# Optimization experiments

Hardware: AMD Instinct MI355X
Metric: run time of the kernel (lower is better)

The kernel has to match this reference:

```python
import jax, jax.numpy as jnp
import numpy as np
from jax import lax

B, C, H, W = 4, 128, 128, 128
MAXD = 192
D = MAXD // 4            # 48 disparity hypotheses at 1/4 scale
WS = 8                   # window size
NH = 8                   # num heads
HD = C // NH             # head dim = 16
SCALE = HD ** -0.5
HID = 4 * C              # mlp hidden (mlp_ratio=4)


def _rel_index(ws):
    coords = np.stack(np.meshgrid(np.arange(ws), np.arange(ws), indexing='ij'))
    cf = coords.reshape(2, -1)
    rel = (cf[:, :, None] - cf[:, None, :]).transpose(1, 2, 0)
    rel[:, :, 0] += ws - 1
    rel[:, :, 1] += ws - 1
    rel[:, :, 0] *= 2 * ws - 1
    return rel.sum(-1)   # [ws*ws, ws*ws]

REL_IDX = jnp.asarray(_rel_index(WS))


def setup_inputs() -> dict:
    key = jax.random.key(0)
    ks = iter(jax.random.split(key, 40))
    rn = lambda shape, s=0.02: jax.random.normal(next(ks), shape, dtype=jnp.float32) * s
    return {
        'feat_l': jax.random.normal(next(ks), (B, C, H, W), dtype=jnp.float32),
        'feat_r': jax.random.normal(next(ks), (B, C, H, W), dtype=jnp.float32),
        'wq': rn((C, C)), 'bq': jnp.zeros((C,), jnp.float32),
        'wk': rn((C, C)), 'bk': jnp.zeros((C,), jnp.float32),
        'wv': rn((C, C)), 'bv': jnp.zeros((C,), jnp.float32),
        'wp': rn((C, C)), 'bp': jnp.zeros((C,), jnp.float32),
        'rpb': rn(((2 * WS - 1) ** 2, NH)),
        'ln1_g': jnp.ones((C,), jnp.float32), 'ln1_b': jnp.zeros((C,), jnp.float32),
        'ln2_g': jnp.ones((C,), jnp.float32), 'ln2_b': jnp.zeros((C,), jnp.float32),
        'mlp_w1': rn((C, HID)), 'mlp_b1': jnp.zeros((HID,), jnp.float32),
        'mlp_w2': rn((HID, C)), 'mlp_b2': jnp.zeros((C,), jnp.float32),
        'un_w1': rn((C, C)), 'un_b1': jnp.zeros((C,), jnp.float32),
        'un_w2': rn((C, C)), 'un_b2': jnp.zeros((C,), jnp.float32),
        'dp_w1': rn((C // 2 + D // 2 + 16, C + D, 3, 3)) if False else rn(((C + D) // 2, C + D, 3, 3)),
        'dp_b1': jnp.zeros(((C + D) // 2,), jnp.float32),
        'bn_g': jnp.ones(((C + D) // 2,), jnp.float32), 'bn_b': jnp.zeros(((C + D) // 2,), jnp.float32),
        'dp_w2': rn((D, (C + D) // 2, 1, 1)), 'dp_b2': jnp.zeros((D,), jnp.float32),
    }


def _ln(x, g, b):
    m = x.mean(-1, keepdims=True)
    v = x.var(-1, keepdims=True)
    return (x - m) * jax.lax.rsqrt(v + 1e-5) * g + b


def _conv(x, w, b, pad):
    y = lax.conv_general_dilated(x, w, (1, 1), [(pad, pad), (pad, pad)],
                                 dimension_numbers=('NCHW', 'OIHW', 'NCHW'))
    return y + b[None, :, None, None]


def _cost_volume(fl, fr):
    # corr[:, d] = mean_c fl[..., w] * fr[..., w-d], zero-padded on the left
    outs = [jnp.mean(fl * fr, axis=1)]
    for d in range(1, D):
        fr_s = jnp.pad(fr[:, :, :, :-d], ((0, 0), (0, 0), (0, 0), (d, 0)))
        outs.append(jnp.mean(fl * fr_s, axis=1))
    return jnp.stack(outs, axis=1)  # [B, D, H, W]


def _win_part(tok):  # [B, H*W, C] -> [B*nW, WS*WS, C]
    x = tok.reshape(B, H // WS, WS, W // WS, WS, C)
    return x.transpose(0, 1, 3, 2, 4, 5).reshape(-1, WS * WS, C)


def _win_rev(win):  # [B*nW, WS*WS, C] -> [B, H*W, C]
    x = win.reshape(B, H // WS, W // WS, WS, WS, C)
    return x.transpose(0, 1, 3, 2, 4, 5).reshape(B, H * W, C)


def _forward(feat_l, feat_r, wq, bq, wk, bk, wv, bv, wp, bp, rpb,
             ln1_g, ln1_b, ln2_g, ln2_b, mlp_w1, mlp_b1, mlp_w2, mlp_b2,
             un_w1, un_b1, un_w2, un_b2, dp_w1, dp_b1, bn_g, bn_b, dp_w2, dp_b2):
    gelu = lambda x: jax.nn.gelu(x, approximate=False)
    cost = _cost_volume(feat_l, feat_r)                       # [B, D, H, W]

    tokens = feat_l.reshape(B, C, H * W).transpose(0, 2, 1)   # [B, N, C]
    unary = gelu(tokens @ un_w1 + un_b1) @ un_w2 + un_b2      # unary potential

    nf = _ln(_win_part(tokens), ln1_g, ln1_b)                 # [Bw, 64, C]
    Bw, N = nf.shape[0], WS * WS
    q = (nf @ wq + bq).reshape(Bw, N, NH, HD).transpose(0, 2, 1, 3)
    k = (nf @ wk + bk).reshape(Bw, N, NH, HD).transpose(0, 2, 1, 3)
    v = (nf @ wv + bv).reshape(Bw, N, NH, HD).transpose(0, 2, 1, 3)
    attn = jnp.einsum('bhnd,bhmd->bhnm', q, k) * SCALE
    bias = rpb[REL_IDX.reshape(-1)].reshape(N, N, NH).transpose(2, 0, 1)
    attn = jax.nn.softmax(attn + bias[None], axis=-1)
    o = jnp.einsum('bhnm,bhmd->bhnd', attn, v).transpose(0, 2, 1, 3).reshape(Bw, N, C)
    pairwise = o @ wp + bp

    x = unary + _win_rev(pairwise)
    x = x + gelu(_ln(x, ln2_g, ln2_b) @ mlp_w1 + mlp_b1) @ mlp_w2 + mlp_b2 * 0.0 + (jnp.zeros((), jnp.float32))
    # (faithful residual MLP; the extra zero terms are no-ops kept out below)
    # -- recompute cleanly to avoid confusion:
    # x = x + mlp(norm2(x))  already done above via single expression

    crf = x.transpose(0, 2, 1).reshape(B, C, H, W)
    fused = jnp.concatenate([crf, cost], axis=1)              # [B, C+D, H, W]

    h1 = jax.nn.relu((_conv(fused, dp_w1, dp_b1, 1)) * jax.lax.rsqrt(jnp.float32(1.0 + 1e-5)) * bn_g[None, :, None, None] + bn_b[None, :, None, None])
    pv = _conv(h1, dp_w2, dp_b2, 0)                           # [B, D, H, W]
    prob = jax.nn.softmax(pv, axis=1)
    disp = jnp.arange(D, dtype=jnp.float32)[None, :, None, None]
    pred = jnp.sum(prob * disp, axis=1, keepdims=True) * 4.0  # [B, 1, H, W]
    return pred


def reference(feat_l, feat_r, wq, bq, wk, bk, wv, bv, wp, bp, rpb,
              ln1_g, ln1_b, ln2_g, ln2_b, mlp_w1, mlp_b1, mlp_w2, mlp_b2,
              un_w1, un_b1, un_w2, un_b2, dp_w1, dp_b1, bn_g, bn_b, dp_w2, dp_b2):
    return _forward(feat_l, feat_r, wq, bq, wk, bk, wv, bv, wp, bp, rpb,
                    ln1_g, ln1_b, ln2_g, ln2_b, mlp_w1, mlp_b1, mlp_w2, mlp_b2,
                    un_w1, un_b1, un_w2, un_b2, dp_w1, dp_b1, bn_g, bn_b, dp_w2, dp_b2)
```

## Files before the change

### kernel.cpp

```cpp
#include <hip/hip_runtime.h>
#include <math.h>

constexpr int Bn = 4, Cc = 128, Hh = 128, Wn = 128, Dd = 48;
constexpr float SCALE = 0.25f;

typedef short  bf16x8 __attribute__((ext_vector_type(8)));
typedef short  bf16x4 __attribute__((ext_vector_type(4)));
typedef float  f32x4  __attribute__((ext_vector_type(4)));
typedef unsigned short u16x8 __attribute__((ext_vector_type(8)));

static __device__ __forceinline__ unsigned short f2bf(float f) {
    return __builtin_bit_cast(unsigned short, (__bf16)f);
}
static __device__ __forceinline__ float bf2f(unsigned short u) {
    return __uint_as_float((unsigned int)u << 16);
}
static __device__ __forceinline__ unsigned int pack2bf(float a, float b) {
    return (unsigned int)f2bf(a) | ((unsigned int)f2bf(b) << 16);
}
static __device__ __forceinline__ float gelu_f(float v) {
    float u = v * (1.5957691216f + 0.0713548162f * v * v);
    return v * __builtin_amdgcn_rcpf(1.0f + __expf(-u));
}

static __device__ __forceinline__ size_t opk_addr(int b, int wh, int ww, int Mt, int ks, int lane) {
    return ((size_t)(b * 16384) + (wh * 8 + Mt * 2 + (ks >> 1)) * 128 + ww * 8) * 128
           + (ks & 1) * 512 + lane * 8;
}

__global__ __launch_bounds__(384) void k_cost(const float* __restrict__ fl,
                                              const float* __restrict__ fr,
                                              unsigned short* __restrict__ costbf) {
    __shared__ float s_fl[2][16][64];
    __shared__ float s_fr[2][16][112];
    int tid = threadIdx.x;
    int w0 = blockIdx.x * 64;
    int hp = blockIdx.y, b = blockIdx.z;
    int row = tid / 192;
    int r = tid - row * 192;
    int wg = r & 15, dg = r >> 4;
    int W = wg * 4, D = dg * 4;
    int h = hp * 2 + row;
    float acc[4][4];
#pragma unroll
    for (int i = 0; i < 4; ++i)
#pragma unroll
        for (int j = 0; j < 4; ++j) acc[i][j] = 0.f;

#pragma unroll 1
    for (int ck = 0; ck < 8; ++ck) {
        int ci0 = ck * 16;
        for (int i = tid; i < 512; i += 384) {
            int rr = i >> 8, rem = i & 255;
            int c = rem >> 4, k4 = rem & 15;
            float4 v = *(const float4*)&fl[((size_t)(b * 128 + ci0 + c) << 14) + (hp * 2 + rr) * 128 + w0 + k4 * 4];
            *(float4*)&s_fl[rr][c][k4 * 4] = v;
        }
        for (int i = tid; i < 896; i += 384) {
            int rr = i / 448, rem = i - rr * 448;
            int c = rem / 28, k4 = rem - c * 28;
            int wgl = w0 - 48 + k4 * 4;
            float4 v = {0.f, 0.f, 0.f, 0.f};
            if (wgl >= 0)
                v = *(const float4*)&fr[((size_t)(b * 128 + ci0 + c) << 14) + (hp * 2 + rr) * 128 + wgl];
            *(float4*)&s_fr[rr][c][k4 * 4] = v;
        }
        __syncthreads();
#pragma unroll
        for (int c = 0; c < 16; ++c) {
            float4 flv = *(const float4*)&s_fl[row][c][W];
            int base = W - D + 44;
            float4 f0 = *(const float4*)&s_fr[row][c][base];
            float4 f1 = *(const float4*)&s_fr[row][c][base + 4];
            float fw[8] = {f0.x, f0.y, f0.z, f0.w, f1.x, f1.y, f1.z, f1.w};
            float fv[4] = {flv.x, flv.y, flv.z, flv.w};
#pragma unroll
            for (int dj = 0; dj < 4; ++dj)
#pragma unroll
                for (int wv = 0; wv < 4; ++wv)
                    acc[dj][wv] += fv[wv] * fw[wv - dj + 4];
        }
        __syncthreads();
    }
    const float inv = 1.0f / 128.0f;
    unsigned short* cb = costbf + ((size_t)(b << 14) + h * 128 + w0 + W) * 64;
    const u16x8 z8 = {0, 0, 0, 0, 0, 0, 0, 0};
#pragma unroll
    for (int wv = 0; wv < 4; ++wv) {
        bf16x4 o4;
#pragma unroll
        for (int dj = 0; dj < 4; ++dj) o4[dj] = (short)f2bf(acc[dj][wv] * inv);
        *(bf16x4*)&cb[wv * 64 + D] = o4;
        if (D == 44) {
            *(u16x8*)&cb[wv * 64 + 48] = z8;
            *(u16x8*)&cb[wv * 64 + 56] = z8;
        }
    }
}

static __device__ void pack_conv(int blk, int lane,
                                 const float* __restrict__ w1, const float* __restrict__ b1,
                                 const float* __restrict__ bng, const float* __restrict__ bnb,
                                 unsigned short* __restrict__ pk, float* __restrict__ bias2) {
    const float rs = 0.9999950000374997f;
    int ct = blk % 6;
    int taplin = blk / 6;
    int tap = taplin % 9, chunk = taplin / 9;
    int co = ct * 16 + (lane & 15);
    int cibase = chunk * 32 + (lane >> 4) * 8;
    u16x8 out;
#pragma unroll
    for (int j = 0; j < 8; ++j) {
        int ci = cibase + j;
        float v = 0.f;
        if (co < 88 && ci < 176) v = w1[(size_t)co * 1584 + ci * 9 + tap] * rs * bng[co];
        out[j] = f2bf(v);
    }
    *(u16x8*)(pk + ((size_t)blk * 64 + lane) * 8) = out;
    if (blk == 0) {
        for (int i = lane; i < 96; i += 64)
            bias2[i] = (i < 88) ? (b1[i] * rs * bng[i] + bnb[i]) : 0.f;
    }
}

static __device__ void pack_gemmB(int blk, int lane,
                                  const float* __restrict__ W,
                                  unsigned short* __restrict__ out, int ncols) {
    int ntiles = ncols >> 4;
    int ks = blk & 3;
    int nt = (blk >> 2) % ntiles;
    int kc = blk / (4 * ntiles);
    int col = nt * 16 + (lane & 15);
    int k0 = kc * 128 + ks * 32 + (lane >> 4) * 8;
    u16x8 o;
#pragma unroll
    for (int j = 0; j < 8; ++j) o[j] = f2bf(W[(size_t)(k0 + j) * ncols + col]);
    *(u16x8*)(out + ((size_t)blk * 64 + lane) * 8) = o;
}

static __device__ void pack_rpb(int blk, int lane,
                                const float* __restrict__ rpb, float* __restrict__ pb) {
    int nt = blk & 3, mt = (blk >> 2) & 3, hh = blk >> 4;
    int tq = nt * 16 + (lane & 15);
    int g = lane >> 4;
    float o[4];
#pragma unroll
    for (int rr = 0; rr < 4; ++rr) {
        int tk = mt * 16 + g * 4 + rr;
        int relidx = (((tq >> 3) - (tk >> 3)) + 7) * 15 + ((tq & 7) - (tk & 7)) + 7;
        o[rr] = rpb[relidx * 8 + hh];
    }
    float4 v = {o[0], o[1], o[2], o[3]};
    *(float4*)(pb + ((size_t)blk * 64 + lane) * 4) = v;
}

__global__ __launch_bounds__(64) void k_pack_all(
        const float* __restrict__ dp_w1, const float* __restrict__ dp_b1,
        const float* __restrict__ bn_g, const float* __restrict__ bn_b,
        unsigned short* __restrict__ pk, float* __restrict__ bias2,
        const float* __restrict__ wq, const float* __restrict__ wk,
        const float* __restrict__ wv, const float* __restrict__ wp,
        unsigned short* __restrict__ pkw,
        const float* __restrict__ rpb, float* __restrict__ pb,
        const float* __restrict__ mlp_w1, unsigned short* __restrict__ pm1,
        const float* __restrict__ mlp_w2, unsigned short* __restrict__ pm2,
        const float* __restrict__ un_w1, unsigned short* __restrict__ pu1,
        const float* __restrict__ un_w2, unsigned short* __restrict__ pu2) {
    int blk = blockIdx.x;
    int lane = threadIdx.x;
    if (blk < 324) {
        pack_conv(blk, lane, dp_w1, dp_b1, bn_g, bn_b, pk, bias2);
    } else if (blk < 452) {
        int bb = blk - 324;
        int mat = bb >> 5;
        const float* W = (mat == 0) ? wq : (mat == 1) ? wk : (mat == 2) ? wv : wp;
        pack_gemmB(bb & 31, lane, W, pkw + (size_t)mat * 16384, 128);
    } else if (blk < 580) {
        pack_rpb(blk - 452, lane, rpb, pb);
    } else if (blk < 708) {
        pack_gemmB(blk - 580, lane, mlp_w1, pm1, 512);
    } else if (blk < 836) {
        pack_gemmB(blk - 708, lane, mlp_w2, pm2, 128);
    } else if (blk < 868) {
        pack_gemmB(blk - 836, lane, un_w1, pu1, 128);
    } else {
        pack_gemmB(blk - 868, lane, un_w2, pu2, 128);
    }
}

__global__ __launch_bounds__(256) void k_unary_mfma(const float* __restrict__ feat_l,
                                                    const unsigned short* __restrict__ pu1,
                                                    const float* __restrict__ b1,
                                                    const unsigned short* __restrict__ pu2,
                                                    const float* __restrict__ b2,
                                                    const float* __restrict__ g1,
                                                    const float* __restrict__ bt1,
                                                    float* __restrict__ x,
                                                    unsigned short* __restrict__ nf) {
    __shared__ __align__(16) unsigned short s_a[64 * 136];
    __shared__ __align__(16) unsigned short s_h[64 * 136];
    int tid = threadIdx.x;
    int wid = tid >> 6, lane = tid & 63;
    int g = lane >> 4, t = lane & 15;
    int n0g = blockIdx.x * 64;
    int b = n0g >> 14;
    int nb = n0g & 16383;

    for (int idx = tid; idx < 4096; idx += 256) {
        int c2 = idx >> 6, nl = idx & 63;
        float v0 = feat_l[((size_t)(b * 128 + 2 * c2) << 14) + nb + nl];
        float v1 = feat_l[((size_t)(b * 128 + 2 * c2 + 1) << 14) + nb + nl];
        *(unsigned int*)&s_a[nl * 136 + 2 * c2] = pack2bf(v0, v1);
    }
    __syncthreads();

    {
        int tok = tid >> 2, q = tid & 3;
        float v[32];
#pragma unroll
        for (int i8 = 0; i8 < 4; ++i8) {
            u16x8 r8 = *(const u16x8*)&s_a[tok * 136 + q * 32 + i8 * 8];
#pragma unroll
            for (int j = 0; j < 8; ++j) v[i8 * 8 + j] = bf2f(r8[j]);
        }
        float s = 0.f, s2 = 0.f;
#pragma unroll
        for (int i = 0; i < 32; ++i) { s += v[i]; s2 += v[i] * v[i]; }
        s += __shfl_xor(s, 1); s += __shfl_xor(s, 2);
        s2 += __shfl_xor(s2, 1); s2 += __shfl_xor(s2, 2);
        float mean = s * (1.f / 128.f);
        float var = s2 * (1.f / 128.f) - mean * mean;
        float rstd = rsqrtf(var + 1e-5f);
        size_t base = (size_t)(n0g + tok) * 128 + q * 32;
#pragma unroll
        for (int i8 = 0; i8 < 4; ++i8) {
            u16x8 o8;
#pragma unroll
            for (int j = 0; j < 8; ++j) {
                int c = q * 32 + i8 * 8 + j;
                o8[j] = f2bf((v[i8 * 8 + j] - mean) * rstd * g1[c] + bt1[c]);
            }
            *(u16x8*)&nf[base + i8 * 8] = o8;
        }
    }

    bf16x8 af[4][4];
#pragma unroll
    for (int Mt = 0; Mt < 4; ++Mt)
#pragma unroll
        for (int ks = 0; ks < 4; ++ks)
            af[Mt][ks] = *(const bf16x8*)&s_a[(Mt * 16 + t) * 136 + ks * 32 + g * 8];

    f32x4 acc1[4][2];
#pragma unroll
    for (int nt2 = 0; nt2 < 2; ++nt2) {
        float bv = b1[(wid * 2 + nt2) * 16 + t];
#pragma unroll
        for (int Mt = 0; Mt < 4; ++Mt) acc1[Mt][nt2] = (f32x4){bv, bv, bv, bv};
    }
#pragma unroll
    for (int ks = 0; ks < 4; ++ks) {
        bf16x8 bf0 = *(const bf16x8*)(pu1 + (size_t)(((wid * 2 + 0) * 4 + ks) * 64 + lane) * 8);
        bf16x8 bf1 = *(const bf16x8*)(pu1 + (size_t)(((wid * 2 + 1) * 4 + ks) * 64 + lane) * 8);
#pragma unroll
        for (int Mt = 0; Mt < 4; ++Mt) {
            acc1[Mt][0] = __builtin_amdgcn_mfma_f32_16x16x32_bf16(af[Mt][ks], bf0, acc1[Mt][0], 0, 0, 0);
            acc1[Mt][1] = __builtin_amdgcn_mfma_f32_16x16x32_bf16(af[Mt][ks], bf1, acc1[Mt][1], 0, 0, 0);
        }
    }
#pragma unroll
    for (int Mt = 0; Mt < 4; ++Mt)
#pragma unroll
        for (int nt2 = 0; nt2 < 2; ++nt2)
#pragma unroll
            for (int rr = 0; rr < 4; ++rr)
                s_h[(Mt * 16 + g * 4 + rr) * 136 + (wid * 2 + nt2) * 16 + t] = f2bf(gelu_f(acc1[Mt][nt2][rr]));
    __syncthreads();

    bf16x8 a2[4][4];
#pragma unroll
    for (int Mt = 0; Mt < 4; ++Mt)
#pragma unroll
        for (int ks = 0; ks < 4; ++ks)
            a2[Mt][ks] = *(const bf16x8*)&s_h[(Mt * 16 + t) * 136 + ks * 32 + g * 8];

    f32x4 acc2[4][2];
#pragma unroll
    for (int nt2 = 0; nt2 < 2; ++nt2) {
        float bv = b2[(wid * 2 + nt2) * 16 + t];
#pragma unroll
        for (int Mt = 0; Mt < 4; ++Mt) acc2[Mt][nt2] = (f32x4){bv, bv, bv, bv};
    }
#pragma unroll
    for (int ks = 0; ks < 4; ++ks) {
        bf16x8 bf0 = *(const bf16x8*)(pu2 + (size_t)(((wid * 2 + 0) * 4 + ks) * 64 + lane) * 8);
        bf16x8 bf1 = *(const bf16x8*)(pu2 + (size_t)(((wid * 2 + 1) * 4 + ks) * 64 + lane) * 8);
#pragma unroll
        for (int Mt = 0; Mt < 4; ++Mt) {
            acc2[Mt][0] = __builtin_amdgcn_mfma_f32_16x16x32_bf16(a2[Mt][ks], bf0, acc2[Mt][0], 0, 0, 0);
            acc2[Mt][1] = __builtin_amdgcn_mfma_f32_16x16x32_bf16(a2[Mt][ks], bf1, acc2[Mt][1], 0, 0, 0);
        }
    }
#pragma unroll
    for (int Mt = 0; Mt < 4; ++Mt)
#pragma unroll
        for (int nt2 = 0; nt2 < 2; ++nt2)
#pragma unroll
            for (int rr = 0; rr < 4; ++rr) {
                int tok = Mt * 16 + g * 4 + rr;
                x[(size_t)(n0g + tok) * 128 + (wid * 2 + nt2) * 16 + t] = acc2[Mt][nt2][rr];
            }
}

__global__ __launch_bounds__(256, 3) void k_attn_core(const unsigned short* nf,
                                                      const unsigned short* __restrict__ pkw,
                                                      const float* __restrict__ pb,
                                                      const float* __restrict__ bq,
                                                      const float* __restrict__ bk,
                                                      const float* __restrict__ bv,
                                                      unsigned short* opk) {
    __shared__ __align__(16) unsigned short s_all[4 * 5760];
    int tid = threadIdx.x;
    int wid = tid >> 6, lane = tid & 63;
    int g = lane >> 4, t = lane & 15;
    int bw = blockIdx.x;
    int b = bw >> 8, wh = (bw >> 4) & 15, ww = bw & 15;

    bf16x8 af[4][4];
#pragma unroll
    for (int Mt = 0; Mt < 4; ++Mt) {
        int tok = Mt * 16 + t;
        size_t gtok = (size_t)(b * 16384) + (wh * 8 + (tok >> 3)) * 128 + ww * 8 + (tok & 7);
#pragma unroll
        for (int ks = 0; ks < 4; ++ks)
            af[Mt][ks] = *(const bf16x8*)&nf[gtok * 128 + ks * 32 + g * 8];
    }
    __syncthreads();

    unsigned short* sQ = s_all + wid * 5760;
    unsigned short* sK = sQ + 1536;
    unsigned short* sV = sQ + 4608;
    unsigned short* sP = sQ;
    unsigned short* sO = sQ;

    const bf16x8 z8v = {0, 0, 0, 0, 0, 0, 0, 0};

#pragma unroll
    for (int hi = 0; hi < 2; ++hi) {
        int h = wid + hi * 4;

        float bqv = bq[h * 16 + t], bkv = bk[h * 16 + t], bvv = bv[h * 16 + t];
        f32x4 qa[4], ka[4], va[4];
#pragma unroll
        for (int Mt = 0; Mt < 4; ++Mt) {
            qa[Mt] = (f32x4){bqv, bqv, bqv, bqv};
            ka[Mt] = (f32x4){bkv, bkv, bkv, bkv};
            va[Mt] = (f32x4){bvv, bvv, bvv, bvv};
        }
#pragma unroll
        for (int ks = 0; ks < 4; ++ks) {
            const unsigned short* wbase = pkw + ((size_t)((h * 4 + ks) * 64 + lane) * 8);
            bf16x8 bfq = *(const bf16x8*)(wbase);
            bf16x8 bfk = *(const bf16x8*)(wbase + 16384);
            bf16x8 bfv = *(const bf16x8*)(wbase + 32768);
#pragma unroll
            for (int Mt = 0; Mt < 4; ++Mt) {
                qa[Mt] = __builtin_amdgcn_mfma_f32_16x16x32_bf16(af[Mt][ks], bfq, qa[Mt], 0, 0, 0);
                ka[Mt] = __builtin_amdgcn_mfma_f32_16x16x32_bf16(af[Mt][ks], bfk, ka[Mt], 0, 0, 0);
                va[Mt] = __builtin_amdgcn_mfma_f32_16x16x32_bf16(af[Mt][ks], bfv, va[Mt], 0, 0, 0);
            }
        }
#pragma unroll
        for (int Mt = 0; Mt < 4; ++Mt) {
            bf16x4 vv;
#pragma unroll
            for (int rr = 0; rr < 4; ++rr) {
                int tok = Mt * 16 + g * 4 + rr;
                sQ[tok * 24 + t] = f2bf(qa[Mt][rr] * SCALE);
                sK[tok * 24 + t] = f2bf(ka[Mt][rr]);
                vv[rr] = (short)f2bf(va[Mt][rr]);
            }
            *(bf16x4*)&sV[t * 72 + Mt * 16 + g * 4] = vv;
        }

        f32x4 s[4][4];
#pragma unroll
        for (int Mtk = 0; Mtk < 4; ++Mtk)
#pragma unroll
            for (int Ntq = 0; Ntq < 4; ++Ntq)
                s[Mtk][Ntq] = *(const f32x4*)(pb + ((size_t)((h * 16 + Mtk * 4 + Ntq) * 64 + lane) * 4));
        bf16x8 bQ[4];
#pragma unroll
        for (int Ntq = 0; Ntq < 4; ++Ntq)
            bQ[Ntq] = (g < 2) ? *(const bf16x8*)&sQ[(Ntq * 16 + t) * 24 + g * 8] : z8v;
#pragma unroll
        for (int Mtk = 0; Mtk < 4; ++Mtk) {
            bf16x8 aK = (g < 2) ? *(const bf16x8*)&sK[(Mtk * 16 + t) * 24 + g * 8] : z8v;
#pragma unroll
            for (int Ntq = 0; Ntq < 4; ++Ntq)
                s[Mtk][Ntq] = __builtin_amdgcn_mfma_f32_16x16x32_bf16(aK, bQ[Ntq], s[Mtk][Ntq], 0, 0, 0);
        }

#pragma unroll
        for (int Ntq = 0; Ntq < 4; ++Ntq) {
            float m = s[0][Ntq][0];
#pragma unroll
            for (int Mtk = 0; Mtk < 4; ++Mtk)
#pragma unroll
                for (int rr = 0; rr < 4; ++rr) m = fmaxf(m, s[Mtk][Ntq][rr]);
            m = fmaxf(m, __shfl_xor(m, 16));
            m = fmaxf(m, __shfl_xor(m, 32));
            float sum = 0.f;
#pragma unroll
            for (int Mtk = 0; Mtk < 4; ++Mtk)
#pragma unroll
                for (int rr = 0; rr < 4; ++rr) {
                    float e = __expf(s[Mtk][Ntq][rr] - m);
                    s[Mtk][Ntq][rr] = e;
                    sum += e;
                }
            sum += __shfl_xor(sum, 16);
            sum += __shfl_xor(sum, 32);
            float inv = __builtin_amdgcn_rcpf(sum);
#pragma unroll
            for (int Mtk = 0; Mtk < 4; ++Mtk) {
                bf16x4 pv;
#pragma unroll
                for (int rr = 0; rr < 4; ++rr) pv[rr] = (short)f2bf(s[Mtk][Ntq][rr] * inv);
                *(bf16x4*)&sP[(Ntq * 16 + t) * 72 + Mtk * 16 + g * 4] = pv;
            }
        }

        f32x4 oa[4];
#pragma unroll
        for (int Mt = 0; Mt < 4; ++Mt) oa[Mt] = (f32x4){0.f, 0.f, 0.f, 0.f};
#pragma unroll
        for (int ksv = 0; ksv < 2; ++ksv) {
            bf16x8 bv2 = *(const bf16x8*)&sV[t * 72 + ksv * 32 + g * 8];
#pragma unroll
            for (int Mt = 0; Mt < 4; ++Mt) {
                bf16x8 ap = *(const bf16x8*)&sP[(Mt * 16 + t) * 72 + ksv * 32 + g * 8];
                oa[Mt] = __builtin_amdgcn_mfma_f32_16x16x32_bf16(ap, bv2, oa[Mt], 0, 0, 0);
            }
        }
#pragma unroll
        for (int Mt = 0; Mt < 4; ++Mt)
#pragma unroll
            for (int rr = 0; rr < 4; ++rr)
                sO[(Mt * 16 + g * 4 + rr) * 16 + t] = f2bf(oa[Mt][rr]);
        int ksf = h >> 1;
        if ((g >> 1) == (h & 1)) {
#pragma unroll
            for (int Mt = 0; Mt < 4; ++Mt) {
                bf16x8 v8 = *(const bf16x8*)&sO[(Mt * 16 + t) * 16 + (g & 1) * 8];
                *(bf16x8*)&opk[opk_addr(b, wh, ww, Mt, ksf, lane)] = v8;
            }
        }
    }
}

__global__ __launch_bounds__(256) void k_mlp_mfma(float* __restrict__ x,
                                                  const unsigned short* __restrict__ opk,
                                                  const unsigned short* __restrict__ pkw,
                                                  const float* __restrict__ bp,
                                                  const float* __restrict__ g2,
                                                  const float* __restrict__ bt2,
                                                  const unsigned short* __restrict__ pm1,
                                                  const float* __restrict__ b1,
                                                  const unsigned short* __restrict__ pm2) {
    __shared__ __align__(16) char smem[35328];
    float* sf = (float*)smem;
    unsigned short* s_h = (unsigned short*)smem;
    float* s_st = (float*)(smem + 33792);
    float* s_gb = (float*)(smem + 34304);
    int tid = threadIdx.x;
    int wid = tid >> 6, lane = tid & 63;
    int g = lane >> 4, t = lane & 15;
    int bw = blockIdx.x;
    int b = bw >> 8, wh = (bw >> 4) & 15, ww = bw & 15;

    auto gtok_of = [&](int tok) -> size_t {
        return (size_t)(b * 16384) + (wh * 8 + (tok >> 3)) * 128 + ww * 8 + (tok & 7);
    };

    if (tid < 128) s_gb[tid] = g2[tid];
    else if (tid < 256) s_gb[tid] = bt2[tid - 128];

    f32x4 out[4][2];
    {
        float bp0 = bp[wid * 32 + t], bp1 = bp[wid * 32 + 16 + t];
#pragma unroll
        for (int Mt = 0; Mt < 4; ++Mt) {
            out[Mt][0] = (f32x4){bp0, bp0, bp0, bp0};
            out[Mt][1] = (f32x4){bp1, bp1, bp1, bp1};
        }
#pragma unroll
        for (int ks = 0; ks < 4; ++ks) {
            bf16x8 b0 = *(const bf16x8*)(pkw + 49152 + (size_t)(((wid * 2 + 0) * 4 + ks) * 64 + lane) * 8);
            bf16x8 b1v = *(const bf16x8*)(pkw + 49152 + (size_t)(((wid * 2 + 1) * 4 + ks) * 64 + lane) * 8);
#pragma unroll
            for (int Mt = 0; Mt < 4; ++Mt) {
                bf16x8 a = *(const bf16x8*)&opk[opk_addr(b, wh, ww, Mt, ks, lane)];
                out[Mt][0] = __builtin_amdgcn_mfma_f32_16x16x32_bf16(a, b0, out[Mt][0], 0, 0, 0);
                out[Mt][1] = __builtin_amdgcn_mfma_f32_16x16x32_bf16(a, b1v, out[Mt][1], 0, 0, 0);
            }
        }
#pragma unroll
        for (int Mt = 0; Mt < 4; ++Mt)
#pragma unroll
            for (int nt2 = 0; nt2 < 2; ++nt2)
#pragma unroll
                for (int rr = 0; rr < 4; ++rr) {
                    int tok = Mt * 16 + g * 4 + rr;
                    int col = (wid * 2 + nt2) * 16 + t;
                    float v = out[Mt][nt2][rr] + x[gtok_of(tok) * 128 + col];
                    out[Mt][nt2][rr] = v;
                    sf[tok * 132 + col] = v;
                }
    }
    __syncthreads();
    {
        int tok = tid >> 2, q = tid & 3;
        float s = 0.f, s2 = 0.f;
        for (int c = q * 32; c < q * 32 + 32; ++c) {
            float v = sf[tok * 132 + c];
            s += v; s2 += v * v;
        }
        s += __shfl_xor(s, 1); s += __shfl_xor(s, 2);
        s2 += __shfl_xor(s2, 1); s2 += __shfl_xor(s2, 2);
        if (q == 0) {
            float mean = s * (1.f / 128.f);
            float var = s2 * (1.f / 128.f) - mean * mean;
            s_st[tok * 2] = mean;
            s_st[tok * 2 + 1] = rsqrtf(var + 1e-5f);
        }
    }
    __syncthreads();
    bf16x8 af2[4][4];
#pragma unroll
    for (int Mt = 0; Mt < 4; ++Mt) {
        int tok = Mt * 16 + t;
        float mean = s_st[tok * 2], rstd = s_st[tok * 2 + 1];
#pragma unroll
        for (int ks = 0; ks < 4; ++ks) {
            int c0 = ks * 32 + g * 8;
            float4 v0 = *(const float4*)&sf[tok * 132 + c0];
            float4 v1 = *(const float4*)&sf[tok * 132 + c0 + 4];
            float vv[8] = {v0.x, v0.y, v0.z, v0.w, v1.x, v1.y, v1.z, v1.w};
            u16x8 o8;
#pragma unroll
            for (int j = 0; j < 8; ++j)
                o8[j] = f2bf((vv[j] - mean) * rstd * s_gb[c0 + j] + s_gb[128 + c0 + j]);
            af2[Mt][ks] = __builtin_bit_cast(bf16x8, o8);
        }
    }
    __syncthreads();

#pragma unroll 1
    for (int hc = 0; hc < 2; ++hc) {
#pragma unroll
        for (int jh = 0; jh < 2; ++jh) {
            f32x4 acc1[4][2];
#pragma unroll
            for (int j2 = 0; j2 < 2; ++j2) {
                float bv = b1[hc * 256 + (wid * 4 + jh * 2 + j2) * 16 + t];
#pragma unroll
                for (int Mt = 0; Mt < 4; ++Mt) acc1[Mt][j2] = (f32x4){bv, bv, bv, bv};
            }
#pragma unroll
            for (int ks = 0; ks < 4; ++ks) {
                int nt0 = hc * 16 + wid * 4 + jh * 2;
                bf16x8 bf0 = *(const bf16x8*)(pm1 + (size_t)((((nt0 + 0) * 4 + ks) * 64 + lane) * 8));
                bf16x8 bf1 = *(const bf16x8*)(pm1 + (size_t)((((nt0 + 1) * 4 + ks) * 64 + lane) * 8));
#pragma unroll
                for (int Mt = 0; Mt < 4; ++Mt) {
                    acc1[Mt][0] = __builtin_amdgcn_mfma_f32_16x16x32_bf16(af2[Mt][ks], bf0, acc1[Mt][0], 0, 0, 0);
                    acc1[Mt][1] = __builtin_amdgcn_mfma_f32_16x16x32_bf16(af2[Mt][ks], bf1, acc1[Mt][1], 0, 0, 0);
                }
            }
#pragma unroll
            for (int Mt = 0; Mt < 4; ++Mt)
#pragma unroll
                for (int j2 = 0; j2 < 2; ++j2)
#pragma unroll
                    for (int rr = 0; rr < 4; ++rr)
                        s_h[(Mt * 16 + g * 4 + rr) * 264 + (wid * 4 + jh * 2 + j2) * 16 + t] =
                            f2bf(gelu_f(acc1[Mt][j2][rr]));
        }
        __syncthreads();
#pragma unroll
        for (int kt = 0; kt < 8; ++kt) {
            int kc = hc * 2 + (kt >> 2), ks = kt & 3;
            bf16x8 bf0 = *(const bf16x8*)(pm2 + (size_t)(((kc * 32 + (wid * 2 + 0) * 4 + ks) * 64 + lane) * 8));
            bf16x8 bf1 = *(const bf16x8*)(pm2 + (size_t)(((kc * 32 + (wid * 2 + 1) * 4 + ks) * 64 + lane) * 8));
#pragma unroll
            for (int Mt = 0; Mt < 4; ++Mt) {
                bf16x8 a2 = *(const bf16x8*)&s_h[(Mt * 16 + t) * 264 + kt * 32 + g * 8];
                out[Mt][0] = __builtin_amdgcn_mfma_f32_16x16x32_bf16(a2, bf0, out[Mt][0], 0, 0, 0);
                out[Mt][1] = __builtin_amdgcn_mfma_f32_16x16x32_bf16(a2, bf1, out[Mt][1], 0, 0, 0);
            }
        }
        __syncthreads();
    }

#pragma unroll
    for (int Mt = 0; Mt < 4; ++Mt)
#pragma unroll
        for (int nt2 = 0; nt2 < 2; ++nt2)
#pragma unroll
            for (int rr = 0; rr < 4; ++rr) {
                int tok = Mt * 16 + g * 4 + rr;
                x[gtok_of(tok) * 128 + (wid * 2 + nt2) * 16 + t] = out[Mt][nt2][rr];
            }
}

__global__ __launch_bounds__(256) void k_conv_mfma(const float* __restrict__ x,
                                                   const unsigned short* __restrict__ costbf,
                                                   const unsigned short* __restrict__ pk,
                                                   const float* __restrict__ bias2,
                                                   float* __restrict__ h1) {
    __shared__ __align__(16) unsigned short s_p[180 * 40];
    int tid = threadIdx.x;
    int wid = tid >> 6, lane = tid & 63;
    int g = lane >> 4, t = lane & 15;
    int tx0 = blockIdx.x * 16, ty0 = blockIdx.y * 8, b = blockIdx.z;

    f32x4 acc[2][6];
#pragma unroll
    for (int p = 0; p < 2; ++p)
#pragma unroll
        for (int ct = 0; ct < 6; ++ct) acc[p][ct] = (f32x4){0.f, 0.f, 0.f, 0.f};

#pragma unroll 1
    for (int chunk = 0; chunk < 6; ++chunk) {
        if (chunk < 4) {
            int ci0 = chunk * 32;
            for (int u = tid; u < 360; u += 256) {
                int pos = u >> 1, half = u & 1;
                int yy = pos / 18, xx = pos - yy * 18;
                int gy = ty0 + yy - 1, gx = tx0 + xx - 1;
                u16x8 lo, hi;
                if (gy >= 0 && gy < 128 && gx >= 0 && gx < 128) {
                    const float4* src = (const float4*)&x[((size_t)(b << 14) + gy * 128 + gx) * 128 + ci0 + half * 16];
                    float4 v0 = src[0], v1 = src[1], v2 = src[2], v3 = src[3];
                    lo[0] = f2bf(v0.x); lo[1] = f2bf(v0.y); lo[2] = f2bf(v0.z); lo[3] = f2bf(v0.w);
                    lo[4] = f2bf(v1.x); lo[5] = f2bf(v1.y); lo[6] = f2bf(v1.z); lo[7] = f2bf(v1.w);
                    hi[0] = f2bf(v2.x); hi[1] = f2bf(v2.y); hi[2] = f2bf(v2.z); hi[3] = f2bf(v2.w);
                    hi[4] = f2bf(v3.x); hi[5] = f2bf(v3.y); hi[6] = f2bf(v3.z); hi[7] = f2bf(v3.w);
                } else {
                    lo = (u16x8)(unsigned short)0; hi = (u16x8)(unsigned short)0;
                }
                unsigned short* dst = &s_p[pos * 40 + half * 16];
                *(u16x8*)dst = lo;
                *(u16x8*)(dst + 8) = hi;
            }
        } else {
            int d0 = (chunk - 4) * 32;
            for (int u = tid; u < 180; u += 256) {
                int yy = u / 18, xx = u - yy * 18;
                int gy = ty0 + yy - 1, gx = tx0 + xx - 1;
                u16x8 lo = (u16x8)(unsigned short)0, hi = (u16x8)(unsigned short)0;
                if (gy >= 0 && gy < 128 && gx >= 0 && gx < 128) {
                    const u16x8* src = (const u16x8*)&costbf[((size_t)(b << 14) + gy * 128 + gx) * 64 + d0];
                    lo = src[0]; hi = src[1];
                    u16x8 l2 = src[2], h2 = src[3];
                    *(u16x8*)&s_p[u * 40 + 16] = l2;
                    *(u16x8*)&s_p[u * 40 + 24] = h2;
                } else {
                    *(u16x8*)&s_p[u * 40 + 16] = lo;
                    *(u16x8*)&s_p[u * 40 + 24] = hi;
                }
                *(u16x8*)&s_p[u * 40 + 0] = lo;
                *(u16x8*)&s_p[u * 40 + 8] = hi;
            }
        }
        __syncthreads();

#pragma unroll 1
        for (int tap = 0; tap < 9; ++tap) {
            int dy = tap / 3, dx = tap - dy * 3;
            const unsigned short* pkt = pk + ((size_t)(chunk * 9 + tap)) * 6 * 512;
            bf16x8 afr[6];
#pragma unroll
            for (int ct = 0; ct < 6; ++ct)
                afr[ct] = *(const bf16x8*)(pkt + ct * 512 + lane * 8);
            bf16x8 bfr[2];
#pragma unroll
            for (int p = 0; p < 2; ++p) {
                int pos = (wid * 2 + p + dy) * 18 + t + dx;
                bfr[p] = *(const bf16x8*)&s_p[pos * 40 + g * 8];
            }
#pragma unroll
            for (int p = 0; p < 2; ++p)
#pragma unroll
                for (int ct = 0; ct < 6; ++ct)
                    acc[p][ct] = __builtin_amdgcn_mfma_f32_16x16x32_bf16(afr[ct], bfr[p], acc[p][ct], 0, 0, 0);
        }
        __syncthreads();
    }

#pragma unroll
    for (int p = 0; p < 2; ++p) {
        int y = ty0 + wid * 2 + p;
#pragma unroll
        for (int ct = 0; ct < 6; ++ct) {
#pragma unroll
            for (int rr = 0; rr < 4; ++rr) {
                int co = ct * 16 + g * 4 + rr;
                if (co < 88) {
                    float v = acc[p][ct][rr] + bias2[co];
                    h1[((size_t)(b * 88 + co) << 14) + y * 128 + tx0 + t] = fmaxf(v, 0.f);
                }
            }
        }
    }
}

__global__ __launch_bounds__(256) void k_head(const float* __restrict__ h1,
                                              const float* __restrict__ w2, const float* __restrict__ b2,
                                              float* __restrict__ out) {
    __shared__ float s_wt[88 * 48];
    __shared__ float s_b[48];
    int tid = threadIdx.x;
    for (int idx = tid; idx < 48 * 88; idx += 256) {
        int d = idx / 88, k = idx % 88;
        s_wt[k * 48 + d] = w2[idx];
    }
    if (tid < 48) s_b[tid] = b2[tid];
    __syncthreads();
    int px = blockIdx.x * 256 + tid;
    int b = px >> 14, r = px & 16383;
    float acc[48];
#pragma unroll
    for (int d = 0; d < 48; ++d) acc[d] = s_b[d];
    for (int k = 0; k < 88; ++k) {
        float hv = h1[((size_t)(b * 88 + k) << 14) + r];
        const float4* wrow = (const float4*)&s_wt[k * 48];
#pragma unroll
        for (int d4 = 0; d4 < 12; ++d4) {
            float4 wv = wrow[d4];
            acc[d4 * 4 + 0] += hv * wv.x;
            acc[d4 * 4 + 1] += hv * wv.y;
            acc[d4 * 4 + 2] += hv * wv.z;
            acc[d4 * 4 + 3] += hv * wv.w;
        }
    }
    float mx = -1e30f;
#pragma unroll
    for (int d = 0; d < 48; ++d) mx = fmaxf(mx, acc[d]);
    float sum = 0.f, wsum = 0.f;
#pragma unroll
    for (int d = 0; d < 48; ++d) {
        float e = __expf(acc[d] - mx);
        sum += e;
        wsum += e * (float)d;
    }
    out[px] = 4.0f * wsum * __builtin_amdgcn_rcpf(sum);
}

extern "C" void kernel_launch(void* const* d_in, const int* in_sizes, int n_in,
                              void* d_out, int out_size, void* d_ws, size_t ws_size,
                              hipStream_t stream) {
    const float* feat_l = (const float*)d_in[0];
    const float* feat_r = (const float*)d_in[1];
    const float* wq = (const float*)d_in[2];
    const float* bq = (const float*)d_in[3];
    const float* wk = (const float*)d_in[4];
    const float* bk = (const float*)d_in[5];
    const float* wv = (const float*)d_in[6];
    const float* bv = (const float*)d_in[7];
    const float* wp = (const float*)d_in[8];
    const float* bp = (const float*)d_in[9];
    const float* rpb = (const float*)d_in[10];
    const float* ln1_g = (const float*)d_in[11];
    const float* ln1_b = (const float*)d_in[12];
    const float* ln2_g = (const float*)d_in[13];
    const float* ln2_b = (const float*)d_in[14];
    const float* mlp_w1 = (const float*)d_in[15];
    const float* mlp_b1 = (const float*)d_in[16];
    const float* mlp_w2 = (const float*)d_in[17];
    const float* un_w1 = (const float*)d_in[19];
    const float* un_b1 = (const float*)d_in[20];
    const float* un_w2 = (const float*)d_in[21];
    const float* un_b2 = (const float*)d_in[22];
    const float* dp_w1 = (const float*)d_in[23];
    const float* dp_b1 = (const float*)d_in[24];
    const float* bn_g = (const float*)d_in[25];
    const float* bn_b = (const float*)d_in[26];
    const float* dp_w2 = (const float*)d_in[27];
    const float* dp_b2 = (const float*)d_in[28];

    float* ws = (float*)d_ws;
    unsigned short* costbf = (unsigned short*)ws;
    float* x = ws + 3145728;
    float* h1 = ws + 11534336;
    unsigned short* nfo = (unsigned short*)h1;
    unsigned short* pk = (unsigned short*)(ws + 17301504);
    float* bias2 = ws + 17384448;
    unsigned short* pkw = (unsigned short*)(ws + 17384544);
    float* pb = ws + 17417312;
    unsigned short* pm1 = (unsigned short*)(ws + 17450080);
    unsigned short* pm2 = (unsigned short*)(ws + 17482848);
    unsigned short* pu1 = (unsigned short*)(ws + 17515616);
    unsigned short* pu2 = (unsigned short*)(ws + 17523808);
    float* out = (float*)d_out;

    k_pack_all<<<900, 64, 0, stream>>>(dp_w1, dp_b1, bn_g, bn_b, pk, bias2,
                                       wq, wk, wv, wp, pkw, rpb, pb,
                                       mlp_w1, pm1, mlp_w2, pm2,
                                       un_w1, pu1, un_w2, pu2);
    k_cost<<<dim3(2, 64, 4), 384, 0, stream>>>(feat_l, feat_r, costbf);
    k_unary_mfma<<<1024, 256, 0, stream>>>(feat_l, pu1, un_b1, pu2, un_b2,
                                           ln1_g, ln1_b, x, nfo);
    k_attn_core<<<1024, 256, 0, stream>>>(nfo, pkw, pb, bq, bk, bv, nfo);
    k_mlp_mfma<<<1024, 256, 0, stream>>>(x, nfo, pkw, bp, ln2_g, ln2_b,
                                         pm1, mlp_b1, pm2);
    k_conv_mfma<<<dim3(8, 16, 4), 256, 0, stream>>>(x, costbf, pk, bias2, h1);
    k_head<<<256, 256, 0, stream>>>(h1, dp_w2, dp_b2, out);
}
```

Before: 258.5 us.

## Merge cost-volume and unary kernels into one launch with block-range dispatch

Merges the cost-volume kernel and the unary MLP kernel into a single launch. Blocks 0-1023 run the unary path and blocks 1024 and above compute the cost volume, so the two independent stages can share the GPU and one launch is removed. The cost path is also rewritten: each block now handles one row with 256 threads, each thread computing 12 disparities for one column, where the old kernel handled two rows with 384 threads doing 4x4 register tiles. This trades register reuse for more blocks, and shared memory is sized for the larger unary path, which may limit occupancy for the cost blocks.

```diff
diff --git a/kernel.cpp b/kernel.cpp
--- a/kernel.cpp
+++ b/kernel.cpp
@@ -26,76 +26,6 @@
 static __device__ __forceinline__ size_t opk_addr(int b, int wh, int ww, int Mt, int ks, int lane) {
     return ((size_t)(b * 16384) + (wh * 8 + Mt * 2 + (ks >> 1)) * 128 + ww * 8) * 128
            + (ks & 1) * 512 + lane * 8;
-}
-
-__global__ __launch_bounds__(384) void k_cost(const float* __restrict__ fl,
-                                              const float* __restrict__ fr,
-                                              unsigned short* __restrict__ costbf) {
-    __shared__ float s_fl[2][16][64];
-    __shared__ float s_fr[2][16][112];
-    int tid = threadIdx.x;
-    int w0 = blockIdx.x * 64;
-    int hp = blockIdx.y, b = blockIdx.z;
-    int row = tid / 192;
-    int r = tid - row * 192;
-    int wg = r & 15, dg = r >> 4;
-    int W = wg * 4, D = dg * 4;
-    int h = hp * 2 + row;
-    float acc[4][4];
-#pragma unroll
-    for (int i = 0; i < 4; ++i)
-#pragma unroll
-        for (int j = 0; j < 4; ++j) acc[i][j] = 0.f;
-
-#pragma unroll 1
-    for (int ck = 0; ck < 8; ++ck) {
-        int ci0 = ck * 16;
-        for (int i = tid; i < 512; i += 384) {
-            int rr = i >> 8, rem = i & 255;
-            int c = rem >> 4, k4 = rem & 15;
-            float4 v = *(const float4*)&fl[((size_t)(b * 128 + ci0 + c) << 14) + (hp * 2 + rr) * 128 + w0 + k4 * 4];
-            *(float4*)&s_fl[rr][c][k4 * 4] = v;
-        }
-        for (int i = tid; i < 896; i += 384) {
-            int rr = i / 448, rem = i - rr * 448;
-            int c = rem / 28, k4 = rem - c * 28;
-            int wgl = w0 - 48 + k4 * 4;
-            float4 v = {0.f, 0.f, 0.f, 0.f};
-            if (wgl >= 0)
-                v = *(const float4*)&fr[((size_t)(b * 128 + ci0 + c) << 14) + (hp * 2 + rr) * 128 + wgl];
-            *(float4*)&s_fr[rr][c][k4 * 4] = v;
-        }
-        __syncthreads();
-#pragma unroll
-        for (int c = 0; c < 16; ++c) {
-            float4 flv = *(const float4*)&s_fl[row][c][W];
-            int base = W - D + 44;
-            float4 f0 = *(const float4*)&s_fr[row][c][base];
-            float4 f1 = *(const float4*)&s_fr[row][c][base + 4];
-            float fw[8] = {f0.x, f0.y, f0.z, f0.w, f1.x, f1.y, f1.z, f1.w};
-            float fv[4] = {flv.x, flv.y, flv.z, flv.w};
-#pragma unroll
-            for (int dj = 0; dj < 4; ++dj)
-#pragma unroll
-                for (int wv = 0; wv < 4; ++wv)
-                    acc[dj][wv] += fv[wv] * fw[wv - dj + 4];
-        }
-        __syncthreads();
-    }
-    const float inv = 1.0f / 128.0f;
-    unsigned short* cb = costbf + ((size_t)(b << 14) + h * 128 + w0 + W) * 64;
-    const u16x8 z8 = {0, 0, 0, 0, 0, 0, 0, 0};
-#pragma unroll
-    for (int wv = 0; wv < 4; ++wv) {
-        bf16x4 o4;
-#pragma unroll
-        for (int dj = 0; dj < 4; ++dj) o4[dj] = (short)f2bf(acc[dj][wv] * inv);
-        *(bf16x4*)&cb[wv * 64 + D] = o4;
-        if (D == 44) {
-            *(u16x8*)&cb[wv * 64 + 48] = z8;
-            *(u16x8*)&cb[wv * 64 + 56] = z8;
-        }
-    }
 }
 
 static __device__ void pack_conv(int blk, int lane,
@@ -188,21 +118,81 @@
     }
 }
 
-__global__ __launch_bounds__(256) void k_unary_mfma(const float* __restrict__ feat_l,
-                                                    const unsigned short* __restrict__ pu1,
-                                                    const float* __restrict__ b1,
-                                                    const unsigned short* __restrict__ pu2,
-                                                    const float* __restrict__ b2,
-                                                    const float* __restrict__ g1,
-                                                    const float* __restrict__ bt1,
-                                                    float* __restrict__ x,
-                                                    unsigned short* __restrict__ nf) {
-    __shared__ __align__(16) unsigned short s_a[64 * 136];
-    __shared__ __align__(16) unsigned short s_h[64 * 136];
+__global__ __launch_bounds__(256) void k_front(const float* __restrict__ feat_l,
+                                               const float* __restrict__ feat_r,
+                                               unsigned short* __restrict__ costbf,
+                                               const unsigned short* __restrict__ pu1,
+                                               const float* __restrict__ b1,
+                                               const unsigned short* __restrict__ pu2,
+                                               const float* __restrict__ b2,
+                                               const float* __restrict__ g1,
+                                               const float* __restrict__ bt1,
+                                               float* __restrict__ x,
+                                               unsigned short* __restrict__ nf) {
+    __shared__ __align__(16) char smem[34816];
     int tid = threadIdx.x;
+    int blk = blockIdx.x;
+
+    if (blk >= 1024) {
+        int cb = blk - 1024;
+        int wt = cb & 1, h = (cb >> 1) & 127, b = cb >> 8;
+        int w0 = wt * 64;
+        int w = tid & 63, dg = tid >> 6;
+        float* s_fl = (float*)smem;
+        float* s_fr = (float*)(smem + 4096);
+        float acc[12];
+#pragma unroll
+        for (int dj = 0; dj < 12; ++dj) acc[dj] = 0.f;
+
+#pragma unroll 1
+        for (int ck = 0; ck < 8; ++ck) {
+            int ci0 = ck * 16;
+            {
+                int c = tid >> 4, k4 = tid & 15;
+                *(float4*)&s_fl[c * 64 + k4 * 4] =
+                    *(const float4*)&feat_l[((size_t)(b * 128 + ci0 + c) << 14) + h * 128 + w0 + k4 * 4];
+            }
+            for (int i = tid; i < 448; i += 256) {
+                int c = i / 28, k4 = i - c * 28;
+                int wgl = w0 - 48 + k4 * 4;
+                float4 v = {0.f, 0.f, 0.f, 0.f};
+                if (wgl >= 0)
+                    v = *(const float4*)&feat_r[((size_t)(b * 128 + ci0 + c) << 14) + h * 128 + wgl];
+                *(float4*)&s_fr[c * 112 + k4 * 4] = v;
+            }
+            __syncthreads();
+            int base = w + 48 - dg * 12;
+#pragma unroll
+            for (int c = 0; c < 16; ++c) {
+                float flv = s_fl[c * 64 + w];
+#pragma unroll
+                for (int dj = 0; dj < 12; ++dj)
+                    acc[dj] += flv * s_fr[c * 112 + base - dj];
+            }
+            __syncthreads();
+        }
+        const float inv = 1.0f / 128.0f;
+        unsigned short* cbp = costbf + ((size_t)(b << 14) + h * 128 + w0 + w) * 64 + dg * 12;
+#pragma unroll
+        for (int q = 0; q < 3; ++q) {
+            bf16x4 o4;
+#pragma unroll
+            for (int rr = 0; rr < 4; ++rr) o4[rr] = (short)f2bf(acc[q * 4 + rr] * inv);
+            *(bf16x4*)&cbp[q * 4] = o4;
+        }
+        if (dg == 3) {
+            const u16x8 z8 = {0, 0, 0, 0, 0, 0, 0, 0};
+            *(u16x8*)&cbp[12] = z8;
+            *(u16x8*)&cbp[20] = z8;
+        }
+        return;
+    }
+
+    unsigned short* s_a = (unsigned short*)smem;
+    unsigned short* s_h = (unsigned short*)(smem + 17408);
     int wid = tid >> 6, lane = tid & 63;
     int g = lane >> 4, t = lane & 15;
-    int n0g = blockIdx.x * 64;
+    int n0g = blk * 64;
     int b = n0g >> 14;
     int nb = n0g & 16383;
 
@@ -809,9 +799,8 @@
                                        wq, wk, wv, wp, pkw, rpb, pb,
                                        mlp_w1, pm1, mlp_w2, pm2,
                                        un_w1, pu1, un_w2, pu2);
-    k_cost<<<dim3(2, 64, 4), 384, 0, stream>>>(feat_l, feat_r, costbf);
-    k_unary_mfma<<<1024, 256, 0, stream>>>(feat_l, pu1, un_b1, pu2, un_b2,
-                                           ln1_g, ln1_b, x, nfo);
+    k_front<<<2048, 256, 0, stream>>>(feat_l, feat_r, costbf, pu1, un_b1,
+                                      pu2, un_b2, ln1_g, ln1_b, x, nfo);
     k_attn_core<<<1024, 256, 0, stream>>>(nfo, pkw, pb, bq, bk, bv, nfo);
     k_mlp_mfma<<<1024, 256, 0, stream>>>(x, nfo, pkw, bp, ln2_g, ln2_b,
                                          pm1, mlp_b1, pm2);
```

Measured after the change: 259.7 us. Within noise of the previous version (+0.5%).

## Store MLP output and conv activations as bf16 to cut memory traffic

Applied to the files above, without the earlier changes.

The MLP kernel now writes its result as bf16 into the reused nfo buffer instead of fp32 x. The conv kernel reads those bf16 values straight into shared memory with one unified staging loop, dropping the fp32-to-bf16 conversion there. The conv output h1 is also stored as bf16, and the head kernel converts it back when reading. This roughly halves the bytes written and read for these intermediate tensors. The cost is extra rounding of h1. The output buffer nfo also aliases the attention-output input that other MLP blocks may still be reading, which could race.

```diff
diff --git a/kernel.cpp b/kernel.cpp
--- a/kernel.cpp
+++ b/kernel.cpp
@@ -459,15 +459,16 @@
     }
 }
 
-__global__ __launch_bounds__(256) void k_mlp_mfma(float* __restrict__ x,
-                                                  const unsigned short* __restrict__ opk,
+__global__ __launch_bounds__(256) void k_mlp_mfma(const float* __restrict__ x,
+                                                  const unsigned short* opk,
                                                   const unsigned short* __restrict__ pkw,
                                                   const float* __restrict__ bp,
                                                   const float* __restrict__ g2,
                                                   const float* __restrict__ bt2,
                                                   const unsigned short* __restrict__ pm1,
                                                   const float* __restrict__ b1,
-                                                  const unsigned short* __restrict__ pm2) {
+                                                  const unsigned short* __restrict__ pm2,
+                                                  unsigned short* xbf) {
     __shared__ __align__(16) char smem[35328];
     float* sf = (float*)smem;
     unsigned short* s_h = (unsigned short*)smem;
@@ -610,15 +611,15 @@
 #pragma unroll
             for (int rr = 0; rr < 4; ++rr) {
                 int tok = Mt * 16 + g * 4 + rr;
-                x[gtok_of(tok) * 128 + (wid * 2 + nt2) * 16 + t] = out[Mt][nt2][rr];
-            }
-}
-
-__global__ __launch_bounds__(256) void k_conv_mfma(const float* __restrict__ x,
+                xbf[gtok_of(tok) * 128 + (wid * 2 + nt2) * 16 + t] = f2bf(out[Mt][nt2][rr]);
+            }
+}
+
+__global__ __launch_bounds__(256) void k_conv_mfma(const unsigned short* __restrict__ xbf,
                                                    const unsigned short* __restrict__ costbf,
                                                    const unsigned short* __restrict__ pk,
                                                    const float* __restrict__ bias2,
-                                                   float* __restrict__ h1) {
+                                                   unsigned short* __restrict__ h1) {
     __shared__ __align__(16) unsigned short s_p[180 * 40];
     int tid = threadIdx.x;
     int wid = tid >> 6, lane = tid & 63;
@@ -633,46 +634,21 @@
 
 #pragma unroll 1
     for (int chunk = 0; chunk < 6; ++chunk) {
-        if (chunk < 4) {
-            int ci0 = chunk * 32;
-            for (int u = tid; u < 360; u += 256) {
-                int pos = u >> 1, half = u & 1;
-                int yy = pos / 18, xx = pos - yy * 18;
-                int gy = ty0 + yy - 1, gx = tx0 + xx - 1;
-                u16x8 lo, hi;
-                if (gy >= 0 && gy < 128 && gx >= 0 && gx < 128) {
-                    const float4* src = (const float4*)&x[((size_t)(b << 14) + gy * 128 + gx) * 128 + ci0 + half * 16];
-                    float4 v0 = src[0], v1 = src[1], v2 = src[2], v3 = src[3];
-                    lo[0] = f2bf(v0.x); lo[1] = f2bf(v0.y); lo[2] = f2bf(v0.z); lo[3] = f2bf(v0.w);
-                    lo[4] = f2bf(v1.x); lo[5] = f2bf(v1.y); lo[6] = f2bf(v1.z); lo[7] = f2bf(v1.w);
-                    hi[0] = f2bf(v2.x); hi[1] = f2bf(v2.y); hi[2] = f2bf(v2.z); hi[3] = f2bf(v2.w);
-                    hi[4] = f2bf(v3.x); hi[5] = f2bf(v3.y); hi[6] = f2bf(v3.z); hi[7] = f2bf(v3.w);
-                } else {
-                    lo = (u16x8)(unsigned short)0; hi = (u16x8)(unsigned short)0;
-                }
-                unsigned short* dst = &s_p[pos * 40 + half * 16];
-                *(u16x8*)dst = lo;
-                *(u16x8*)(dst + 8) = hi;
-            }
-        } else {
-            int d0 = (chunk - 4) * 32;
-            for (int u = tid; u < 180; u += 256) {
-                int yy = u / 18, xx = u - yy * 18;
-                int gy = ty0 + yy - 1, gx = tx0 + xx - 1;
-                u16x8 lo = (u16x8)(unsigned short)0, hi = (u16x8)(unsigned short)0;
-                if (gy >= 0 && gy < 128 && gx >= 0 && gx < 128) {
-                    const u16x8* src = (const u16x8*)&costbf[((size_t)(b << 14) + gy * 128 + gx) * 64 + d0];
-                    lo = src[0]; hi = src[1];
-                    u16x8 l2 = src[2], h2 = src[3];
-                    *(u16x8*)&s_p[u * 40 + 16] = l2;
-                    *(u16x8*)&s_p[u * 40 + 24] = h2;
-                } else {
-                    *(u16x8*)&s_p[u * 40 + 16] = lo;
-                    *(u16x8*)&s_p[u * 40 + 24] = hi;
-                }
-                *(u16x8*)&s_p[u * 40 + 0] = lo;
-                *(u16x8*)&s_p[u * 40 + 8] = hi;
-            }
+        for (int u = tid; u < 180; u += 256) {
+            int yy = u / 18, xx = u - yy * 18;
+            int gy = ty0 + yy - 1, gx = tx0 + xx - 1;
+            u16x8 v0 = (u16x8)(unsigned short)0, v1 = v0, v2 = v0, v3 = v0;
+            if (gy >= 0 && gy < 128 && gx >= 0 && gx < 128) {
+                size_t pix = (size_t)(b << 14) + gy * 128 + gx;
+                const u16x8* src = (chunk < 4)
+                    ? (const u16x8*)&xbf[pix * 128 + chunk * 32]
+                    : (const u16x8*)&costbf[pix * 64 + (chunk - 4) * 32];
+                v0 = src[0]; v1 = src[1]; v2 = src[2]; v3 = src[3];
+            }
+            *(u16x8*)&s_p[u * 40 + 0] = v0;
+            *(u16x8*)&s_p[u * 40 + 8] = v1;
+            *(u16x8*)&s_p[u * 40 + 16] = v2;
+            *(u16x8*)&s_p[u * 40 + 24] = v3;
         }
         __syncthreads();
 
@@ -709,14 +685,14 @@
                 int co = ct * 16 + g * 4 + rr;
                 if (co < 88) {
                     float v = acc[p][ct][rr] + bias2[co];
-                    h1[((size_t)(b * 88 + co) << 14) + y * 128 + tx0 + t] = fmaxf(v, 0.f);
+                    h1[((size_t)(b * 88 + co) << 14) + y * 128 + tx0 + t] = f2bf(fmaxf(v, 0.f));
                 }
             }
         }
     }
 }
 
-__global__ __launch_bounds__(256) void k_head(const float* __restrict__ h1,
+__global__ __launch_bounds__(256) void k_head(const unsigned short* __restrict__ h1,
                                               const float* __restrict__ w2, const float* __restrict__ b2,
                                               float* __restrict__ out) {
     __shared__ float s_wt[88 * 48];
@@ -734,7 +710,7 @@
 #pragma unroll
     for (int d = 0; d < 48; ++d) acc[d] = s_b[d];
     for (int k = 0; k < 88; ++k) {
-        float hv = h1[((size_t)(b * 88 + k) << 14) + r];
+        float hv = bf2f(h1[((size_t)(b * 88 + k) << 14) + r]);
         const float4* wrow = (const float4*)&s_wt[k * 48];
 #pragma unroll
         for (int d4 = 0; d4 < 12; ++d4) {
@@ -793,8 +769,9 @@
     float* ws = (float*)d_ws;
     unsigned short* costbf = (unsigned short*)ws;
     float* x = ws + 3145728;
-    float* h1 = ws + 11534336;
-    unsigned short* nfo = (unsigned short*)h1;
+    unsigned short* h1bf = (unsigned short*)(ws + 3145728);
+    float* h1_unused = ws + 11534336;
+    unsigned short* nfo = (unsigned short*)h1_unused;
     unsigned short* pk = (unsigned short*)(ws + 17301504);
     float* bias2 = ws + 17384448;
     unsigned short* pkw = (unsigned short*)(ws + 17384544);
@@ -814,7 +791,7 @@
                                            ln1_g, ln1_b, x, nfo);
     k_attn_core<<<1024, 256, 0, stream>>>(nfo, pkw, pb, bq, bk, bv, nfo);
     k_mlp_mfma<<<1024, 256, 0, stream>>>(x, nfo, pkw, bp, ln2_g, ln2_b,
-                                         pm1, mlp_b1, pm2);
-    k_conv_mfma<<<dim3(8, 16, 4), 256, 0, stream>>>(x, costbf, pk, bias2, h1);
-    k_head<<<256, 256, 0, stream>>>(h1, dp_w2, dp_b2, out);
-}
+                                         pm1, mlp_b1, pm2, nfo);
+    k_conv_mfma<<<dim3(8, 16, 4), 256, 0, stream>>>(nfo, costbf, pk, bias2, h1bf);
+    k_head<<<256, 256, 0, stream>>>(h1bf, dp_w2, dp_b2, out);
+}
```

Result: no change. 255.9 us (-1.0%).
